# Performance work log

Measured on AMD Instinct MI355X. Metric: run time of the kernel, lower is better.

Reference implementation:

```python
import jax, jax.numpy as jnp
import numpy as np

B, C, H, W = 32, 3, 128, 128
NMIX = 10  # 10 logistic mixture components -> 100 param channels for RGB


def setup_inputs() -> dict:
    key = jax.random.key(0)
    k1, k2 = jax.random.split(key)
    samples = jax.random.uniform(k1, (B, C, H, W), dtype=jnp.float32)  # pixel values in [0,1]
    params = jax.random.normal(k2, (B, 10 * NMIX, H, W), dtype=jnp.float32)  # PixelCNN output params
    return {"samples": samples, "params": params}


def _discretized_mix_logistic_log_prob(x, l):
    # x: [B,H,W,3] in [-1,1]; l: [B,H,W,100]
    logit_probs = l[..., :NMIX]                                   # [B,H,W,NMIX]
    rest = l[..., NMIX:].reshape(l.shape[0], l.shape[1], l.shape[2], 3, 3 * NMIX)
    means = rest[..., :NMIX]                                      # [B,H,W,3,NMIX]
    log_scales = jnp.maximum(rest[..., NMIX:2 * NMIX], -7.0)
    coeffs = jnp.tanh(rest[..., 2 * NMIX:3 * NMIX])

    x0 = x[..., 0:1]  # [B,H,W,1]
    x1 = x[..., 1:2]
    m1 = means[..., 0, :]
    m2 = means[..., 1, :] + coeffs[..., 0, :] * x0
    m3 = means[..., 2, :] + coeffs[..., 1, :] * x0 + coeffs[..., 2, :] * x1
    means_c = jnp.stack([m1, m2, m3], axis=3)                     # [B,H,W,3,NMIX]

    xb = x[..., None]                                             # [B,H,W,3,1]
    centered = xb - means_c
    inv_stdv = jnp.exp(-log_scales)
    plus_in = inv_stdv * (centered + 1.0 / 255.0)
    min_in = inv_stdv * (centered - 1.0 / 255.0)
    cdf_plus = jax.nn.sigmoid(plus_in)
    cdf_min = jax.nn.sigmoid(min_in)
    log_cdf_plus = plus_in - jax.nn.softplus(plus_in)             # log CDF at left edge bin (x = -1)
    log_one_minus_cdf_min = -jax.nn.softplus(min_in)              # log(1-CDF) at right edge bin (x = 1)
    cdf_delta = cdf_plus - cdf_min
    mid_in = inv_stdv * centered
    log_pdf_mid = mid_in - log_scales - 2.0 * jax.nn.softplus(mid_in)

    inner = jnp.where(cdf_delta > 1e-5,
                      jnp.log(jnp.maximum(cdf_delta, 1e-12)),
                      log_pdf_mid - np.float32(np.log(127.5)))
    log_probs_ch = jnp.where(xb < -0.999, log_cdf_plus,
                             jnp.where(xb > 0.999, log_one_minus_cdf_min, inner))
    # sum over channels, mixture weights, logsumexp over mixtures
    log_probs = log_probs_ch.sum(axis=3) + jax.nn.log_softmax(logit_probs, axis=-1)
    return jax.scipy.special.logsumexp(log_probs, axis=-1).sum()


def reference(samples, params):
    # _PixelCNNDistribution.log_prob: rescale samples to [-1,1], evaluate
    # discretized mixture-of-logistics log-likelihood (= -discretized_mix_logistic_loss).
    x = jnp.transpose(samples * 2.0 - 1.0, (0, 2, 3, 1))  # NCHW -> NHWC
    l = jnp.transpose(params, (0, 2, 3, 1))
    return _discretized_mix_logistic_log_prob(x, l)
```

## Files before the change

### kernel.cpp

```cpp
#include <hip/hip_runtime.h>
#include <math.h>

#define HW 16384
#define HW2 8192
#define NMIX 10
#define NPIX (32 * HW)
#define NTHREADS (NPIX / 2)
#define NBLOCKS (NTHREADS / 256)

__device__ __forceinline__ float fexp(float x) { return __expf(x); }
__device__ __forceinline__ float flog(float x) { return __logf(x); }
__device__ __forceinline__ float frcp(float x) { return __builtin_amdgcn_rcpf(x); }

__device__ __forceinline__ float ftanh(float y) {
    float t = fexp(-2.0f * fabsf(y));
    float r = (1.0f - t) * frcp(1.0f + t);
    return (y >= 0.0f) ? r : -r;
}

__device__ __forceinline__ float channel_logprob(float x, float mean, float ls,
                                                 bool waveEdge) {
    const float INV255 = 0.00392156862745098f;
    const float LOG127_5 = 4.852030263919617f;
    float inv = fexp(-ls);
    float centered = x - mean;
    float plus_in = inv * (centered + INV255);
    float min_in  = inv * (centered - INV255);
    float mid_in  = inv * centered;

    float tp = fexp(-fabsf(plus_in));
    float rp = frcp(1.0f + tp);
    float sig_plus = (plus_in >= 0.0f) ? rp : tp * rp;

    float tm = fexp(-fabsf(min_in));
    float rm = frcp(1.0f + tm);
    float sig_min = (min_in >= 0.0f) ? rm : tm * rm;

    float cdf_delta = sig_plus - sig_min;

    float tmid = fexp(-fabsf(mid_in));
    float sp_mid = fmaxf(mid_in, 0.0f) + flog(1.0f + tmid);
    float log_pdf_mid = mid_in - ls - 2.0f * sp_mid;

    float r = (cdf_delta > 1e-5f) ? flog(fmaxf(cdf_delta, 1e-12f))
                                  : (log_pdf_mid - LOG127_5);
    if (waveEdge) {
        float sp_plus = fmaxf(plus_in, 0.0f) + flog(1.0f + tp);
        float sp_min  = fmaxf(min_in, 0.0f) + flog(1.0f + tm);
        float log_cdf_plus   = plus_in - sp_plus;
        float log_om_cdf_min = -sp_min;
        r = (x < -0.999f) ? log_cdf_plus
          : ((x > 0.999f) ? log_om_cdf_min : r);
    }
    return r;
}

__device__ __forceinline__ void lse_update(float& m, float& s, float v) {
    float d = v - m;
    float e = fexp(-fabsf(d));
    bool grow = (d > 0.0f);
    s = grow ? (s * e + 1.0f) : (s + e);
    m = grow ? v : m;
}

__global__ __launch_bounds__(256, 4) void pixelcnn_kernel(
    const float2* __restrict__ samples, const float2* __restrict__ params,
    float* __restrict__ out)
{
    int q  = blockIdx.x * blockDim.x + threadIdx.x;
    int b  = q >> 13;
    int hw = q & (HW2 - 1);

    const float2* sp = samples + (size_t)b * 3   * HW2 + hw;
    const float2* pp = params  + (size_t)b * 100 * HW2 + hw;

    float2 s0 = sp[0];
    float2 s1 = sp[HW2];
    float2 s2 = sp[2 * HW2];

    float x0[2] = {2.0f * s0.x - 1.0f, 2.0f * s0.y - 1.0f};
    float x1[2] = {2.0f * s1.x - 1.0f, 2.0f * s1.y - 1.0f};
    float x2[2] = {2.0f * s2.x - 1.0f, 2.0f * s2.y - 1.0f};

    bool edge = false;
    #pragma unroll
    for (int j = 0; j < 2; ++j)
        edge |= (fabsf(x0[j]) > 0.999f) | (fabsf(x1[j]) > 0.999f)
              | (fabsf(x2[j]) > 0.999f);
    bool waveEdge = (__ballot(edge) != 0ULL);

    float mr[2] = {-3.4e38f, -3.4e38f}, sr[2] = {0.0f, 0.0f};
    float ml[2] = {-3.4e38f, -3.4e38f}, sl[2] = {0.0f, 0.0f};

    float2 cur[10], nxt[10];
    #pragma unroll
    for (int f = 0; f < 10; ++f) cur[f] = pp[(size_t)(10 * f) * HW2];

    #pragma unroll 1
    for (int k = 0; k < NMIX; ++k) {
        int kn = (k < NMIX - 1) ? k + 1 : k;
        #pragma unroll
        for (int f = 0; f < 10; ++f) nxt[f] = pp[(size_t)(10 * f + kn) * HW2];

        const float* logit = (const float*)&cur[0];
        const float* mean0 = (const float*)&cur[1];
        const float* lsc0  = (const float*)&cur[2];
        const float* cw0   = (const float*)&cur[3];
        const float* mean1 = (const float*)&cur[4];
        const float* lsc1  = (const float*)&cur[5];
        const float* cw1   = (const float*)&cur[6];
        const float* mean2 = (const float*)&cur[7];
        const float* lsc2  = (const float*)&cur[8];
        const float* cw2   = (const float*)&cur[9];

        #pragma unroll
        for (int j = 0; j < 2; ++j) {
            float ls0 = fmaxf(lsc0[j], -7.0f);
            float ls1 = fmaxf(lsc1[j], -7.0f);
            float ls2 = fmaxf(lsc2[j], -7.0f);
            float c0 = ftanh(cw0[j]);
            float c1 = ftanh(cw1[j]);
            float c2 = ftanh(cw2[j]);

            float m1 = mean0[j];
            float m2 = mean1[j] + c0 * x0[j];
            float m3 = mean2[j] + c1 * x0[j] + c2 * x1[j];

            float lp = channel_logprob(x0[j], m1, ls0, waveEdge)
                     + channel_logprob(x1[j], m2, ls1, waveEdge)
                     + channel_logprob(x2[j], m3, ls2, waveEdge);

            lse_update(mr[j], sr[j], lp + logit[j]);
            lse_update(ml[j], sl[j], logit[j]);
        }

        #pragma unroll
        for (int f = 0; f < 10; ++f) cur[f] = nxt[f];
    }

    float val = 0.0f;
    #pragma unroll
    for (int j = 0; j < 2; ++j)
        val += (mr[j] + flog(sr[j])) - (ml[j] + flog(sl[j]));

    #pragma unroll
    for (int off = 32; off > 0; off >>= 1)
        val += __shfl_down(val, off, 64);

    __shared__ float wsum[4];
    int lane = threadIdx.x & 63;
    int wid  = threadIdx.x >> 6;
    if (lane == 0) wsum[wid] = val;
    __syncthreads();
    if (threadIdx.x == 0) {
        float bsum = (wsum[0] + wsum[1]) + (wsum[2] + wsum[3]);
        atomicAdd(out, bsum);
    }
}

extern "C" void kernel_launch(void* const* d_in, const int* in_sizes, int n_in,
                              void* d_out, int out_size, void* d_ws, size_t ws_size,
                              hipStream_t stream) {
    const float2* samples = (const float2*)d_in[0];
    const float2* params  = (const float2*)d_in[1];
    float* out = (float*)d_out;

    hipMemsetAsync(out, 0, sizeof(float), stream);
    pixelcnn_kernel<<<NBLOCKS, 256, 0, stream>>>(samples, params, out);
}
```

Before: 295.2 us.

## Process four pixels per thread with float4 loads and explicit ping-pong prefetch

Each thread now handles four consecutive pixels using 128-bit float4 loads instead of two pixels with float2 loads, which halves the thread count. The mixture loop is fully unrolled in pairs, with two named register buffers that alternate as prefetch targets, removing the per-iteration register copy. Launch bounds drop to 2 blocks per CU to leave room for the larger register footprint. The aim is wider memory transactions and more loads in flight per thread, at the cost of lower occupancy and higher register pressure.

```diff
diff --git a/kernel.cpp b/kernel.cpp
--- a/kernel.cpp
+++ b/kernel.cpp
@@ -2,11 +2,11 @@
 #include <math.h>
 
 #define HW 16384
-#define HW2 8192
+#define HW4 4096
 #define NMIX 10
 #define NPIX (32 * HW)
-#define NTHREADS (NPIX / 2)
-#define NBLOCKS (NTHREADS / 256)
+#define NQUAD (NPIX / 4)
+#define NBLOCKS (NQUAD / 256)
 
 __device__ __forceinline__ float fexp(float x) { return __expf(x); }
 __device__ __forceinline__ float flog(float x) { return __logf(x); }
@@ -63,84 +63,97 @@
     m = grow ? v : m;
 }
 
-__global__ __launch_bounds__(256, 4) void pixelcnn_kernel(
-    const float2* __restrict__ samples, const float2* __restrict__ params,
+__device__ __forceinline__ void mixture_step(
+    const float4 (&buf)[10],
+    const float (&x0)[4], const float (&x1)[4], const float (&x2)[4],
+    float (&mr)[4], float (&sr)[4], float (&ml)[4], float (&sl)[4],
+    bool waveEdge)
+{
+    const float* logit = (const float*)&buf[0];
+    const float* mean0 = (const float*)&buf[1];
+    const float* lsc0  = (const float*)&buf[2];
+    const float* cw0   = (const float*)&buf[3];
+    const float* mean1 = (const float*)&buf[4];
+    const float* lsc1  = (const float*)&buf[5];
+    const float* cw1   = (const float*)&buf[6];
+    const float* mean2 = (const float*)&buf[7];
+    const float* lsc2  = (const float*)&buf[8];
+    const float* cw2   = (const float*)&buf[9];
+
+    #pragma unroll
+    for (int j = 0; j < 4; ++j) {
+        float ls0 = fmaxf(lsc0[j], -7.0f);
+        float ls1 = fmaxf(lsc1[j], -7.0f);
+        float ls2 = fmaxf(lsc2[j], -7.0f);
+        float c0 = ftanh(cw0[j]);
+        float c1 = ftanh(cw1[j]);
+        float c2 = ftanh(cw2[j]);
+
+        float m1 = mean0[j];
+        float m2 = mean1[j] + c0 * x0[j];
+        float m3 = mean2[j] + c1 * x0[j] + c2 * x1[j];
+
+        float lp = channel_logprob(x0[j], m1, ls0, waveEdge)
+                 + channel_logprob(x1[j], m2, ls1, waveEdge)
+                 + channel_logprob(x2[j], m3, ls2, waveEdge);
+
+        lse_update(mr[j], sr[j], lp + logit[j]);
+        lse_update(ml[j], sl[j], logit[j]);
+    }
+}
+
+__global__ __launch_bounds__(256, 2) void pixelcnn_kernel(
+    const float4* __restrict__ samples, const float4* __restrict__ params,
     float* __restrict__ out)
 {
     int q  = blockIdx.x * blockDim.x + threadIdx.x;
-    int b  = q >> 13;
-    int hw = q & (HW2 - 1);
+    int b  = q >> 12;
+    int hw = q & (HW4 - 1);
 
-    const float2* sp = samples + (size_t)b * 3   * HW2 + hw;
-    const float2* pp = params  + (size_t)b * 100 * HW2 + hw;
+    const float4* sp = samples + (size_t)b * 3   * HW4 + hw;
+    const float4* pp = params  + (size_t)b * 100 * HW4 + hw;
 
-    float2 s0 = sp[0];
-    float2 s1 = sp[HW2];
-    float2 s2 = sp[2 * HW2];
+    float4 s0 = sp[0];
+    float4 s1 = sp[HW4];
+    float4 s2 = sp[2 * HW4];
+    const float* fs0 = (const float*)&s0;
+    const float* fs1 = (const float*)&s1;
+    const float* fs2 = (const float*)&s2;
 
-    float x0[2] = {2.0f * s0.x - 1.0f, 2.0f * s0.y - 1.0f};
-    float x1[2] = {2.0f * s1.x - 1.0f, 2.0f * s1.y - 1.0f};
-    float x2[2] = {2.0f * s2.x - 1.0f, 2.0f * s2.y - 1.0f};
-
+    float x0[4], x1[4], x2[4], mr[4], sr[4], ml[4], sl[4];
     bool edge = false;
     #pragma unroll
-    for (int j = 0; j < 2; ++j)
+    for (int j = 0; j < 4; ++j) {
+        x0[j] = 2.0f * fs0[j] - 1.0f;
+        x1[j] = 2.0f * fs1[j] - 1.0f;
+        x2[j] = 2.0f * fs2[j] - 1.0f;
         edge |= (fabsf(x0[j]) > 0.999f) | (fabsf(x1[j]) > 0.999f)
               | (fabsf(x2[j]) > 0.999f);
+        mr[j] = -3.4e38f; sr[j] = 0.0f;
+        ml[j] = -3.4e38f; sl[j] = 0.0f;
+    }
     bool waveEdge = (__ballot(edge) != 0ULL);
 
-    float mr[2] = {-3.4e38f, -3.4e38f}, sr[2] = {0.0f, 0.0f};
-    float ml[2] = {-3.4e38f, -3.4e38f}, sl[2] = {0.0f, 0.0f};
+    float4 buf0[10], buf1[10];
+    #pragma unroll
+    for (int f = 0; f < 10; ++f) buf0[f] = pp[(size_t)(10 * f) * HW4];
 
-    float2 cur[10], nxt[10];
     #pragma unroll
-    for (int f = 0; f < 10; ++f) cur[f] = pp[(size_t)(10 * f) * HW2];
-
-    #pragma unroll 1
-    for (int k = 0; k < NMIX; ++k) {
-        int kn = (k < NMIX - 1) ? k + 1 : k;
+    for (int kk = 0; kk < NMIX / 2; ++kk) {
+        int k0 = 2 * kk;
         #pragma unroll
-        for (int f = 0; f < 10; ++f) nxt[f] = pp[(size_t)(10 * f + kn) * HW2];
-
-        const float* logit = (const float*)&cur[0];
-        const float* mean0 = (const float*)&cur[1];
-        const float* lsc0  = (const float*)&cur[2];
-        const float* cw0   = (const float*)&cur[3];
-        const float* mean1 = (const float*)&cur[4];
-        const float* lsc1  = (const float*)&cur[5];
-        const float* cw1   = (const float*)&cur[6];
-        const float* mean2 = (const float*)&cur[7];
-        const float* lsc2  = (const float*)&cur[8];
-        const float* cw2   = (const float*)&cur[9];
-
-        #pragma unroll
-        for (int j = 0; j < 2; ++j) {
-            float ls0 = fmaxf(lsc0[j], -7.0f);
-            float ls1 = fmaxf(lsc1[j], -7.0f);
-            float ls2 = fmaxf(lsc2[j], -7.0f);
-            float c0 = ftanh(cw0[j]);
-            float c1 = ftanh(cw1[j]);
-            float c2 = ftanh(cw2[j]);
-
-            float m1 = mean0[j];
-            float m2 = mean1[j] + c0 * x0[j];
-            float m3 = mean2[j] + c1 * x0[j] + c2 * x1[j];
-
-            float lp = channel_logprob(x0[j], m1, ls0, waveEdge)
-                     + channel_logprob(x1[j], m2, ls1, waveEdge)
-                     + channel_logprob(x2[j], m3, ls2, waveEdge);
-
-            lse_update(mr[j], sr[j], lp + logit[j]);
-            lse_update(ml[j], sl[j], logit[j]);
+        for (int f = 0; f < 10; ++f) buf1[f] = pp[(size_t)(10 * f + k0 + 1) * HW4];
+        mixture_step(buf0, x0, x1, x2, mr, sr, ml, sl, waveEdge);
+        if (kk < NMIX / 2 - 1) {
+            #pragma unroll
+            for (int f = 0; f < 10; ++f) buf0[f] = pp[(size_t)(10 * f + k0 + 2) * HW4];
         }
-
-        #pragma unroll
-        for (int f = 0; f < 10; ++f) cur[f] = nxt[f];
+        mixture_step(buf1, x0, x1, x2, mr, sr, ml, sl, waveEdge);
     }
 
     float val = 0.0f;
     #pragma unroll
-    for (int j = 0; j < 2; ++j)
+    for (int j = 0; j < 4; ++j)
         val += (mr[j] + flog(sr[j])) - (ml[j] + flog(sl[j]));
 
     #pragma unroll
@@ -161,8 +174,8 @@
 extern "C" void kernel_launch(void* const* d_in, const int* in_sizes, int n_in,
                               void* d_out, int out_size, void* d_ws, size_t ws_size,
                               hipStream_t stream) {
-    const float2* samples = (const float2*)d_in[0];
-    const float2* params  = (const float2*)d_in[1];
+    const float4* samples = (const float4*)d_in[0];
+    const float4* params  = (const float4*)d_in[1];
     float* out = (float*)d_out;
 
     hipMemsetAsync(out, 0, sizeof(float), stream);
```

After: 315.1 us. 6.7% more time.
